# Performance work log

Hardware: AMD Instinct MI355X
Metric: run time of the kernel (lower is better)

## Reference

```python
import jax, jax.numpy as jnp
import numpy as np

H = 256        # hidden_dim
NH = 8         # num_heads
DH = H // NH   # head_dim
B, L1, L2 = 2, 512, 512


def setup_inputs() -> dict:
    key = jax.random.key(0)
    ks = jax.random.split(key, 8)
    s = 1.0 / np.sqrt(H)
    return {
        "embed1": jax.random.normal(ks[0], (B, L1, H), jnp.float32),
        "embed2": jax.random.normal(ks[1], (B, L2, H), jnp.float32),
        # nn.MultiheadAttention in-projection (packed q,k,v)
        "in_proj_w": jax.random.normal(ks[2], (3 * H, H), jnp.float32) * s,
        "in_proj_b": jax.random.normal(ks[3], (3 * H,), jnp.float32) * 0.01,
        # match_score MLP: Linear(2H -> H), Linear(H -> 1)
        "W1": jax.random.normal(ks[4], (H, 2 * H), jnp.float32) * (1.0 / np.sqrt(2 * H)),
        "b1": jax.random.normal(ks[5], (H,), jnp.float32) * 0.01,
        "W2": jax.random.normal(ks[6], (1, H), jnp.float32) * s,
        "b2": jax.random.normal(ks[7], (1,), jnp.float32) * 0.01,
    }


def reference(embed1, embed2, in_proj_w, in_proj_b, W1, b1, W2, b2):
    # ---- cross-attention weights (head-averaged, torch default) ----
    q = embed1 @ in_proj_w[:H].T + in_proj_b[:H]            # (B,L1,H)
    k = embed2 @ in_proj_w[H:2 * H].T + in_proj_b[H:2 * H]  # (B,L2,H)
    qh = q.reshape(B, L1, NH, DH)
    kh = k.reshape(B, L2, NH, DH)
    scale = 1.0 / np.sqrt(DH)
    logits = jnp.einsum('bqhd,bkhd->bhqk', qh, kh) * scale  # (B,NH,L1,L2)
    attn = jax.nn.softmax(logits, axis=-1)
    attn_weights = attn.mean(axis=1)                        # (B,L1,L2)

    # ---- pairwise MLP scorer: fused broadcast form of cat([e1,e2]) @ W1.T ----
    h1 = embed1 @ W1[:, :H].T                               # (B,L1,H)
    h2 = embed2 @ W1[:, H:].T                               # (B,L2,H)
    h = jax.nn.relu(h1[:, :, None, :] + h2[:, None, :, :] + b1)  # (B,L1,L2,H)
    match_scores = jax.nn.sigmoid(jnp.einsum('bijh,h->bij', h, W2[0]) + b2[0])
    return attn_weights, match_scores
```

## Files before the change

kernel.cpp:

```cpp
#include <hip/hip_runtime.h>
#include <hip/hip_fp16.h>
#include <stdint.h>

typedef _Float16 f16x8 __attribute__((ext_vector_type(8)));
typedef _Float16 f16x2 __attribute__((ext_vector_type(2)));
typedef float f32x4 __attribute__((ext_vector_type(4)));

#define LL 512
#define HH 256

__device__ __forceinline__ unsigned pkrtz(float a, float b){
    return __builtin_bit_cast(unsigned, __builtin_amdgcn_cvt_pkrtz(a, b));
}

#if __has_builtin(__builtin_amdgcn_fdot2)
__device__ __forceinline__ float fdot2(f16x2 x, f16x2 w, float acc){
    return __builtin_amdgcn_fdot2(x, w, acc, false);
}
#else
__device__ __forceinline__ float fdot2(f16x2 x, f16x2 w, float acc){
    return fmaf((float)x[0], (float)w[0], fmaf((float)x[1], (float)w[1], acc));
}
#endif

__global__ __launch_bounds__(256) void k_proj(
    const float* __restrict__ e1, const float* __restrict__ e2,
    const float* __restrict__ ipw, const float* __restrict__ ipb,
    const float* __restrict__ W1, const float* __restrict__ b1,
    _Float16* __restrict__ wq, _Float16* __restrict__ wk,
    _Float16* __restrict__ wh1, _Float16* __restrict__ wh2)
{
    __shared__ __align__(16) _Float16 As[64 * 256];
    __shared__ __align__(16) _Float16 Bs[64 * 256];
    const int t = threadIdx.x;
    const int blk = blockIdx.x;
    const int g = blk >> 6, mt = (blk >> 2) & 15, nt = blk & 3;
    const int m0 = mt * 64, n0 = nt * 64;
    const float* abase = (g == 0 || g == 2) ? e1 : e2;
    const float* bbase; int bstride;
    if (g == 0)      { bbase = ipw;         bstride = 256; }
    else if (g == 1) { bbase = ipw + 65536; bstride = 256; }
    else if (g == 2) { bbase = W1;          bstride = 512; }
    else             { bbase = W1 + 256;    bstride = 512; }

    #pragma unroll
    for (int s = 0; s < 8; s++){
        const int c = s * 256 + t;
        const int row = c >> 5, kg = c & 31;
        const int dst = row * 256 + ((kg ^ (row & 7)) << 3);
        {
            const float4* sa = (const float4*)(abase + (size_t)(m0 + row) * 256 + kg * 8);
            float4 a0 = sa[0], a1 = sa[1];
            uint4 pk = { pkrtz(a0.x, a0.y), pkrtz(a0.z, a0.w),
                         pkrtz(a1.x, a1.y), pkrtz(a1.z, a1.w) };
            *(uint4*)(As + dst) = pk;
        }
        {
            const float4* sb = (const float4*)(bbase + (size_t)(n0 + row) * bstride + kg * 8);
            float4 b0 = sb[0], b1v = sb[1];
            uint4 pk = { pkrtz(b0.x, b0.y), pkrtz(b0.z, b0.w),
                         pkrtz(b1v.x, b1v.y), pkrtz(b1v.z, b1v.w) };
            *(uint4*)(Bs + dst) = pk;
        }
    }
    __syncthreads();
    const int w = t >> 6, l = t & 63;
    const int lr = l & 15, lg = l >> 4;
    f32x4 acc[4] = {};
    const int brow = w * 16 + lr;
    #pragma unroll
    for (int kk = 0; kk < 8; kk++){
        const int cb = ((kk * 4 + lg) ^ (lr & 7)) << 3;
        f16x8 bf = *(const f16x8*)(Bs + brow * 256 + cb);
        #pragma unroll
        for (int ms = 0; ms < 4; ms++){
            f16x8 af = *(const f16x8*)(As + (ms * 16 + lr) * 256 + cb);
            acc[ms] = __builtin_amdgcn_mfma_f32_16x16x32_f16(af, bf, acc[ms], 0, 0, 0);
        }
    }
    const int n = n0 + w * 16 + lr;
    float bias = 0.f, scale = 1.f;
    if (g == 0)      { bias = ipb[n];       scale = 0.17677669529663689f; }
    else if (g == 1) { bias = ipb[256 + n]; }
    else if (g == 3) { bias = b1[n]; }
    _Float16* outp = (g == 0) ? wq : ((g == 1) ? wk : ((g == 2) ? wh1 : wh2));
    #pragma unroll
    for (int ms = 0; ms < 4; ms++)
        #pragma unroll
        for (int r = 0; r < 4; r++){
            const int m = m0 + ms * 16 + lg * 4 + r;
            outp[(size_t)m * 256 + n] = (_Float16)((acc[ms][r] + bias) * scale);
        }
}

__global__ __launch_bounds__(256) void k_logits(
    const _Float16* __restrict__ wq, const _Float16* __restrict__ wk,
    _Float16* __restrict__ lg)
{
    const int t = threadIdx.x;
    const int blk = blockIdx.x;
    const int jt = blk & 7, it = (blk >> 3) & 7, h = (blk >> 6) & 7, b = blk >> 9;
    const int w = t >> 6, l = t & 63, lr = l & 15, lg2 = l >> 4;
    const int i0 = it * 64 + w * 16, j0 = jt * 64;
    const f32x4 zero = {};
    f16x8 af = *(const f16x8*)(wq + (size_t)(b * LL + i0 + lr) * HH + h * 32 + lg2 * 8);
    f32x4 acc[4];
    #pragma unroll
    for (int jb = 0; jb < 4; jb++){
        f16x8 bf = *(const f16x8*)(wk + (size_t)(b * LL + j0 + jb * 16 + lr) * HH + h * 32 + lg2 * 8);
        acc[jb] = __builtin_amdgcn_mfma_f32_16x16x32_f16(af, bf, zero, 0, 0, 0);
    }
    _Float16* orow = lg + ((size_t)(b * 8 + h) * LL + i0 + lg2 * 4) * LL + j0 + lr;
    #pragma unroll
    for (int jb = 0; jb < 4; jb++)
        #pragma unroll
        for (int r = 0; r < 4; r++)
            orow[(size_t)r * LL + jb * 16] = (_Float16)acc[jb][r];
}

__global__ __launch_bounds__(256) void k_smmean(
    const _Float16* __restrict__ lg, float* __restrict__ outA)
{
    __shared__ float ps[4][8];
    __shared__ float inv[8];
    const int t = threadIdx.x;
    const int bi = blockIdx.x;
    const int b = bi >> 9, i = bi & 511;
    const int w = t >> 6;
    const size_t base = (size_t)(b * 8) * LL * LL + (size_t)i * LL + 2 * t;
    float e[8][2], p[8];
    #pragma unroll
    for (int h = 0; h < 8; h++){
        f16x2 u = *(const f16x2*)(lg + base + (size_t)h * LL * LL);
        e[h][0] = __expf((float)u[0]);
        e[h][1] = __expf((float)u[1]);
        p[h] = e[h][0] + e[h][1];
    }
    #pragma unroll
    for (int h = 0; h < 8; h++){
        float s = p[h];
        #pragma unroll
        for (int mask = 1; mask < 64; mask <<= 1) s += __shfl_xor(s, mask, 64);
        if ((t & 63) == 0) ps[w][h] = s;
    }
    __syncthreads();
    if (t < 8) inv[t] = 1.0f / (8.0f * (ps[0][t] + ps[1][t] + ps[2][t] + ps[3][t]));
    __syncthreads();
    float iv[8];
    #pragma unroll
    for (int h = 0; h < 8; h++) iv[h] = inv[h];
    float2 o; o.x = 0.f; o.y = 0.f;
    #pragma unroll
    for (int h = 0; h < 8; h++){
        o.x = fmaf(e[h][0], iv[h], o.x);
        o.y = fmaf(e[h][1], iv[h], o.y);
    }
    *(float2*)(outA + (size_t)bi * LL + 2 * t) = o;
}

__global__ __launch_bounds__(256) void k_match(
    const _Float16* __restrict__ wh1, const _Float16* __restrict__ wh2,
    const float* __restrict__ W2, const float* __restrict__ b2,
    float* __restrict__ outM)
{
    __shared__ __align__(16) _Float16 h1s[64 * 256];
    __shared__ __align__(16) _Float16 h2s[32 * 256];
    __shared__ __align__(16) f16x2 w2s[128];
    const int t = threadIdx.x;
    const int blk = blockIdx.x;
    const int b = blk >> 7, it = (blk >> 4) & 7, jt = blk & 15;
    const int i0 = it * 64, j0 = jt * 32;
    if (t < 128){
        unsigned pk = pkrtz(W2[2 * t], W2[2 * t + 1]);
        w2s[t] = __builtin_bit_cast(f16x2, pk);
    }
    #pragma unroll
    for (int s = 0; s < 8; s++){
        const int c = s * 256 + t;
        const int row = c >> 5, hc = c & 31;
        uint4 v = *(const uint4*)(wh1 + (size_t)(b * LL + i0 + row) * HH + hc * 8);
        *(uint4*)(h1s + row * 256 + ((hc ^ ((row >> 2) & 7)) << 3)) = v;
    }
    #pragma unroll
    for (int s = 0; s < 4; s++){
        const int c = s * 256 + t;
        const int row = c >> 5, hc = c & 31;
        uint4 v = *(const uint4*)(wh2 + (size_t)(b * LL + j0 + row) * HH + hc * 8);
        *(uint4*)(h2s + row * 256 + ((hc ^ ((row >> 1) & 7)) << 3)) = v;
    }
    __syncthreads();
    const int ti = t >> 4, tj = t & 15;
    float acc[4][2] = {};
    for (int hc = 0; hc < 32; hc++){
        unsigned ua[4][4], uc[2][4], uw[4];
        {
            uint4 v;
            #pragma unroll
            for (int rr = 0; rr < 4; rr++){
                v = *(const uint4*)(h1s + (ti * 4 + rr) * 256 + ((hc ^ (ti & 7)) << 3));
                ua[rr][0] = v.x; ua[rr][1] = v.y; ua[rr][2] = v.z; ua[rr][3] = v.w;
            }
            #pragma unroll
            for (int rr = 0; rr < 2; rr++){
                v = *(const uint4*)(h2s + (tj * 2 + rr) * 256 + ((hc ^ (tj & 7)) << 3));
                uc[rr][0] = v.x; uc[rr][1] = v.y; uc[rr][2] = v.z; uc[rr][3] = v.w;
            }
            v = *(const uint4*)(w2s + hc * 4);
            uw[0] = v.x; uw[1] = v.y; uw[2] = v.z; uw[3] = v.w;
        }
        #pragma unroll
        for (int e = 0; e < 4; e++){
            const f16x2 wv = __builtin_bit_cast(f16x2, uw[e]);
            #pragma unroll
            for (int ii = 0; ii < 4; ii++){
                const f16x2 av = __builtin_bit_cast(f16x2, ua[ii][e]);
                #pragma unroll
                for (int jj = 0; jj < 2; jj++){
                    const f16x2 cv = __builtin_bit_cast(f16x2, uc[jj][e]);
                    f16x2 x = av + cv;
                    x = __builtin_elementwise_max(x, (f16x2)((_Float16)0.0f));
                    acc[ii][jj] = fdot2(x, wv, acc[ii][jj]);
                }
            }
        }
    }
    const float bb = b2[0];
    #pragma unroll
    for (int ii = 0; ii < 4; ii++){
        const int i = i0 + ti * 4 + ii;
        float2 o;
        o.x = 1.0f / (1.0f + __expf(-(acc[ii][0] + bb)));
        o.y = 1.0f / (1.0f + __expf(-(acc[ii][1] + bb)));
        *(float2*)(outM + (size_t)(b * LL + i) * LL + j0 + tj * 2) = o;
    }
}

extern "C" void kernel_launch(void* const* d_in, const int* in_sizes, int n_in,
                              void* d_out, int out_size, void* d_ws, size_t ws_size,
                              hipStream_t stream)
{
    const float* e1  = (const float*)d_in[0];
    const float* e2  = (const float*)d_in[1];
    const float* ipw = (const float*)d_in[2];
    const float* ipb = (const float*)d_in[3];
    const float* W1  = (const float*)d_in[4];
    const float* b1  = (const float*)d_in[5];
    const float* W2  = (const float*)d_in[6];
    const float* b2  = (const float*)d_in[7];
    float* outA = (float*)d_out;
    float* outM = outA + (size_t)2 * LL * LL;

    _Float16* ws  = (_Float16*)d_ws;
    _Float16* wq  = ws;
    _Float16* wk  = ws + 262144;
    _Float16* wh1 = ws + 524288;
    _Float16* wh2 = ws + 786432;
    _Float16* lg  = ws + 1048576;

    hipLaunchKernelGGL(k_proj,   dim3(256),  dim3(256), 0, stream,
                       e1, e2, ipw, ipb, W1, b1, wq, wk, wh1, wh2);
    hipLaunchKernelGGL(k_logits, dim3(1024), dim3(256), 0, stream, wq, wk, lg);
    hipLaunchKernelGGL(k_smmean, dim3(1024), dim3(256), 0, stream, lg, outA);
    hipLaunchKernelGGL(k_match,  dim3(256),  dim3(256), 0, stream,
                       wh1, wh2, W2, b2, outM);
}
```

Measured before the change: 97.25 us.

## Fuse attention logits and softmax-mean in LDS; retile match kernel

Merges the logits kernel and the softmax/head-mean kernel into one kernel. Each 512-thread block computes all 8 heads' logits for 16 query rows into padded shared memory, reduces the exp sums, and writes the head-averaged weights directly. This removes the fp16 logits round trip through global memory and one launch, but only 64 blocks cover the GPU and each uses a large shared-memory footprint. Separately, the match kernel is retiled to 32x32 output tiles with 512 blocks and one j per thread, trading register reuse of h2 for more parallelism.

```diff
diff --git a/kernel.cpp b/kernel.cpp
--- a/kernel.cpp
+++ b/kernel.cpp
@@ -8,6 +8,7 @@
 
 #define LL 512
 #define HH 256
+#define LGS 516
 
 __device__ __forceinline__ unsigned pkrtz(float a, float b){
     return __builtin_bit_cast(unsigned, __builtin_amdgcn_cvt_pkrtz(a, b));
@@ -93,69 +94,74 @@
         }
 }
 
-__global__ __launch_bounds__(256) void k_logits(
+__global__ __launch_bounds__(512) void k_attn(
     const _Float16* __restrict__ wq, const _Float16* __restrict__ wk,
-    _Float16* __restrict__ lg)
-{
+    float* __restrict__ outA)
+{
+    __shared__ __align__(16) _Float16 lgs[8 * 16 * LGS];
+    __shared__ float part[8][8][16];
+    __shared__ float inv[8][16];
     const int t = threadIdx.x;
-    const int blk = blockIdx.x;
-    const int jt = blk & 7, it = (blk >> 3) & 7, h = (blk >> 6) & 7, b = blk >> 9;
+    const int b = blockIdx.x >> 5;
+    const int i0 = (blockIdx.x & 31) << 4;
     const int w = t >> 6, l = t & 63, lr = l & 15, lg2 = l >> 4;
-    const int i0 = it * 64 + w * 16, j0 = jt * 64;
+    const int j0 = w * 64;
     const f32x4 zero = {};
-    f16x8 af = *(const f16x8*)(wq + (size_t)(b * LL + i0 + lr) * HH + h * 32 + lg2 * 8);
-    f32x4 acc[4];
-    #pragma unroll
-    for (int jb = 0; jb < 4; jb++){
-        f16x8 bf = *(const f16x8*)(wk + (size_t)(b * LL + j0 + jb * 16 + lr) * HH + h * 32 + lg2 * 8);
-        acc[jb] = __builtin_amdgcn_mfma_f32_16x16x32_f16(af, bf, zero, 0, 0, 0);
-    }
-    _Float16* orow = lg + ((size_t)(b * 8 + h) * LL + i0 + lg2 * 4) * LL + j0 + lr;
-    #pragma unroll
-    for (int jb = 0; jb < 4; jb++)
-        #pragma unroll
-        for (int r = 0; r < 4; r++)
-            orow[(size_t)r * LL + jb * 16] = (_Float16)acc[jb][r];
-}
-
-__global__ __launch_bounds__(256) void k_smmean(
-    const _Float16* __restrict__ lg, float* __restrict__ outA)
-{
-    __shared__ float ps[4][8];
-    __shared__ float inv[8];
-    const int t = threadIdx.x;
-    const int bi = blockIdx.x;
-    const int b = bi >> 9, i = bi & 511;
-    const int w = t >> 6;
-    const size_t base = (size_t)(b * 8) * LL * LL + (size_t)i * LL + 2 * t;
-    float e[8][2], p[8];
-    #pragma unroll
+
     for (int h = 0; h < 8; h++){
-        f16x2 u = *(const f16x2*)(lg + base + (size_t)h * LL * LL);
-        e[h][0] = __expf((float)u[0]);
-        e[h][1] = __expf((float)u[1]);
-        p[h] = e[h][0] + e[h][1];
-    }
-    #pragma unroll
-    for (int h = 0; h < 8; h++){
-        float s = p[h];
-        #pragma unroll
-        for (int mask = 1; mask < 64; mask <<= 1) s += __shfl_xor(s, mask, 64);
-        if ((t & 63) == 0) ps[w][h] = s;
-    }
-    __syncthreads();
-    if (t < 8) inv[t] = 1.0f / (8.0f * (ps[0][t] + ps[1][t] + ps[2][t] + ps[3][t]));
-    __syncthreads();
-    float iv[8];
-    #pragma unroll
-    for (int h = 0; h < 8; h++) iv[h] = inv[h];
-    float2 o; o.x = 0.f; o.y = 0.f;
-    #pragma unroll
-    for (int h = 0; h < 8; h++){
-        o.x = fmaf(e[h][0], iv[h], o.x);
-        o.y = fmaf(e[h][1], iv[h], o.y);
-    }
-    *(float2*)(outA + (size_t)bi * LL + 2 * t) = o;
+        f16x8 q = *(const f16x8*)(wq + (size_t)(b * LL + i0 + lr) * HH + h * 32 + lg2 * 8);
+        float s4[4] = {0.f, 0.f, 0.f, 0.f};
+        #pragma unroll
+        for (int jb = 0; jb < 4; jb++){
+            f16x8 kf = *(const f16x8*)(wk + (size_t)(b * LL + j0 + jb * 16 + lr) * HH + h * 32 + lg2 * 8);
+            f32x4 a = __builtin_amdgcn_mfma_f32_16x16x32_f16(q, kf, zero, 0, 0, 0);
+            #pragma unroll
+            for (int r = 0; r < 4; r++){
+                _Float16 lf = (_Float16)a[r];
+                lgs[(h * 16 + lg2 * 4 + r) * LGS + j0 + jb * 16 + lr] = lf;
+                s4[r] += __expf((float)lf);
+            }
+        }
+        #pragma unroll
+        for (int r = 0; r < 4; r++){
+            #pragma unroll
+            for (int mask = 1; mask < 16; mask <<= 1)
+                s4[r] += __shfl_xor(s4[r], mask, 64);
+        }
+        if (lr == 0){
+            #pragma unroll
+            for (int r = 0; r < 4; r++) part[w][h][lg2 * 4 + r] = s4[r];
+        }
+    }
+    __syncthreads();
+    if (t < 128){
+        const int h = t >> 4, i = t & 15;
+        float s = 0.f;
+        #pragma unroll
+        for (int ww = 0; ww < 8; ww++) s += part[ww][h][i];
+        inv[h][i] = 1.0f / (8.0f * s);
+    }
+    __syncthreads();
+    #pragma unroll
+    for (int dp = 0; dp < 2; dp++){
+        const int ii = w * 2 + dp;
+        float iv[8];
+        #pragma unroll
+        for (int h = 0; h < 8; h++) iv[h] = inv[h][ii];
+        float* orow = outA + (size_t)(b * LL + i0 + ii) * LL;
+        #pragma unroll
+        for (int k = 0; k < 4; k++){
+            const int j = 2 * l + 128 * k;
+            float2 o; o.x = 0.f; o.y = 0.f;
+            #pragma unroll
+            for (int h = 0; h < 8; h++){
+                f16x2 u = *(const f16x2*)(lgs + (h * 16 + ii) * LGS + j);
+                o.x = fmaf(__expf((float)u[0]), iv[h], o.x);
+                o.y = fmaf(__expf((float)u[1]), iv[h], o.y);
+            }
+            *(float2*)(orow + j) = o;
+        }
+    }
 }
 
 __global__ __launch_bounds__(256) void k_match(
@@ -163,75 +169,56 @@
     const float* __restrict__ W2, const float* __restrict__ b2,
     float* __restrict__ outM)
 {
-    __shared__ __align__(16) _Float16 h1s[64 * 256];
+    __shared__ __align__(16) _Float16 h1s[32 * 256];
     __shared__ __align__(16) _Float16 h2s[32 * 256];
     __shared__ __align__(16) f16x2 w2s[128];
     const int t = threadIdx.x;
     const int blk = blockIdx.x;
-    const int b = blk >> 7, it = (blk >> 4) & 7, jt = blk & 15;
-    const int i0 = it * 64, j0 = jt * 32;
+    const int b = blk >> 8, it = (blk >> 4) & 15, jt = blk & 15;
+    const int i0 = it * 32, j0 = jt * 32;
     if (t < 128){
         unsigned pk = pkrtz(W2[2 * t], W2[2 * t + 1]);
         w2s[t] = __builtin_bit_cast(f16x2, pk);
     }
     #pragma unroll
-    for (int s = 0; s < 8; s++){
-        const int c = s * 256 + t;
-        const int row = c >> 5, hc = c & 31;
-        uint4 v = *(const uint4*)(wh1 + (size_t)(b * LL + i0 + row) * HH + hc * 8);
-        *(uint4*)(h1s + row * 256 + ((hc ^ ((row >> 2) & 7)) << 3)) = v;
-    }
-    #pragma unroll
     for (int s = 0; s < 4; s++){
         const int c = s * 256 + t;
         const int row = c >> 5, hc = c & 31;
-        uint4 v = *(const uint4*)(wh2 + (size_t)(b * LL + j0 + row) * HH + hc * 8);
-        *(uint4*)(h2s + row * 256 + ((hc ^ ((row >> 1) & 7)) << 3)) = v;
-    }
-    __syncthreads();
-    const int ti = t >> 4, tj = t & 15;
-    float acc[4][2] = {};
+        const int dst = row * 256 + ((hc ^ (row & 7)) << 3);
+        *(uint4*)(h1s + dst) = *(const uint4*)(wh1 + (size_t)(b * LL + i0 + row) * HH + hc * 8);
+        *(uint4*)(h2s + dst) = *(const uint4*)(wh2 + (size_t)(b * LL + j0 + row) * HH + hc * 8);
+    }
+    __syncthreads();
+    const int ti = t >> 5, tj = t & 31;
+    float acc[4] = {0.f, 0.f, 0.f, 0.f};
+    #pragma unroll 4
     for (int hc = 0; hc < 32; hc++){
-        unsigned ua[4][4], uc[2][4], uw[4];
-        {
-            uint4 v;
-            #pragma unroll
-            for (int rr = 0; rr < 4; rr++){
-                v = *(const uint4*)(h1s + (ti * 4 + rr) * 256 + ((hc ^ (ti & 7)) << 3));
-                ua[rr][0] = v.x; ua[rr][1] = v.y; ua[rr][2] = v.z; ua[rr][3] = v.w;
+        uint4 va[4];
+        #pragma unroll
+        for (int rr = 0; rr < 4; rr++){
+            const int row = ti * 4 + rr;
+            va[rr] = *(const uint4*)(h1s + row * 256 + ((hc ^ (row & 7)) << 3));
+        }
+        uint4 vc = *(const uint4*)(h2s + tj * 256 + ((hc ^ (tj & 7)) << 3));
+        uint4 vw = *(const uint4*)(w2s + hc * 4);
+        const unsigned uc_[4] = {vc.x, vc.y, vc.z, vc.w};
+        const unsigned uw_[4] = {vw.x, vw.y, vw.z, vw.w};
+        #pragma unroll
+        for (int rr = 0; rr < 4; rr++){
+            const unsigned ue[4] = {va[rr].x, va[rr].y, va[rr].z, va[rr].w};
+            #pragma unroll
+            for (int e = 0; e < 4; e++){
+                f16x2 x = __builtin_bit_cast(f16x2, ue[e]) + __builtin_bit_cast(f16x2, uc_[e]);
+                x = __builtin_elementwise_max(x, (f16x2)((_Float16)0.0f));
+                acc[rr] = fdot2(x, __builtin_bit_cast(f16x2, uw_[e]), acc[rr]);
             }
-            #pragma unroll
-            for (int rr = 0; rr < 2; rr++){
-                v = *(const uint4*)(h2s + (tj * 2 + rr) * 256 + ((hc ^ (tj & 7)) << 3));
-                uc[rr][0] = v.x; uc[rr][1] = v.y; uc[rr][2] = v.z; uc[rr][3] = v.w;
-            }
-            v = *(const uint4*)(w2s + hc * 4);
-            uw[0] = v.x; uw[1] = v.y; uw[2] = v.z; uw[3] = v.w;
-        }
-        #pragma unroll
-        for (int e = 0; e < 4; e++){
-            const f16x2 wv = __builtin_bit_cast(f16x2, uw[e]);
-            #pragma unroll
-            for (int ii = 0; ii < 4; ii++){
-                const f16x2 av = __builtin_bit_cast(f16x2, ua[ii][e]);
-                #pragma unroll
-                for (int jj = 0; jj < 2; jj++){
-                    const f16x2 cv = __builtin_bit_cast(f16x2, uc[jj][e]);
-                    f16x2 x = av + cv;
-                    x = __builtin_elementwise_max(x, (f16x2)((_Float16)0.0f));
-                    acc[ii][jj] = fdot2(x, wv, acc[ii][jj]);
-                }
-            }
         }
     }
     const float bb = b2[0];
     #pragma unroll
-    for (int ii = 0; ii < 4; ii++){
-        const int i = i0 + ti * 4 + ii;
-        float2 o;
-        o.x = 1.0f / (1.0f + __expf(-(acc[ii][0] + bb)));
-        o.y = 1.0f / (1.0f + __expf(-(acc[ii][1] + bb)));
-        *(float2*)(outM + (size_t)(b * LL + i) * LL + j0 + tj * 2) = o;
+    for (int rr = 0; rr < 4; rr++){
+        outM[(size_t)(b * LL + i0 + ti * 4 + rr) * LL + j0 + tj] =
+            1.0f / (1.0f + __expf(-(acc[rr] + bb)));
     }
 }
 
@@ -255,12 +242,10 @@
     _Float16* wk  = ws + 262144;
     _Float16* wh1 = ws + 524288;
     _Float16* wh2 = ws + 786432;
-    _Float16* lg  = ws + 1048576;
-
-    hipLaunchKernelGGL(k_proj,   dim3(256),  dim3(256), 0, stream,
+
+    hipLaunchKernelGGL(k_proj,  dim3(256), dim3(256), 0, stream,
                        e1, e2, ipw, ipb, W1, b1, wq, wk, wh1, wh2);
-    hipLaunchKernelGGL(k_logits, dim3(1024), dim3(256), 0, stream, wq, wk, lg);
-    hipLaunchKernelGGL(k_smmean, dim3(1024), dim3(256), 0, stream, lg, outA);
-    hipLaunchKernelGGL(k_match,  dim3(256),  dim3(256), 0, stream,
+    hipLaunchKernelGGL(k_attn,  dim3(64),  dim3(512), 0, stream, wq, wk, outA);
+    hipLaunchKernelGGL(k_match, dim3(512), dim3(256), 0, stream,
                        wh1, wh2, W2, b2, outM);
 }
```

After: 96.35 us. About the same (-0.9%).
